# Performance work log

Hardware: AMD Instinct MI355X
Metric: run time of the kernel (lower is better)

## Reference

```python
import jax, jax.numpy as jnp
import numpy as np

VOCAB = 50257
DIM = 1024
B, S = 4, 4096


def setup_inputs() -> dict:
    key = jax.random.key(0)
    k1, k2, k3 = jax.random.split(key, 3)
    input_ids = jax.random.randint(k1, (B, S), 0, VOCAB)
    weight = jax.random.normal(k2, (VOCAB, DIM), dtype=jnp.float32)
    # R initialized as a random matrix stand-in for the learned Stiefel rotation
    R = jax.random.normal(k3, (DIM, DIM), dtype=jnp.float32) / np.sqrt(DIM)
    return {"input_ids": input_ids, "weight": weight, "R": R}


def reference(input_ids, weight, R):
    # Faithful to the module: rotate the FULL embedding table, then gather.
    w_eff = weight @ R              # [V, D] @ [D, D] -> [V, D]
    return jnp.take(w_eff, input_ids, axis=0)  # [B, S, D]
```

## Files before the change

kernel.cpp:

```cpp
#include <hip/hip_runtime.h>
#include <hip/hip_bf16.h>


typedef __attribute__((ext_vector_type(4))) float f32x4;
typedef __attribute__((ext_vector_type(8))) short s16x8;
typedef __attribute__((ext_vector_type(2))) int i32x2;

#define DIM 1024
#define NT 16

__device__ __forceinline__ short f2bf(float f) {
  unsigned u = __float_as_uint(f);
  unsigned r = (u + 0x7FFFu + ((u >> 16) & 1u)) >> 16;
  return (short)r;
}

__device__ __forceinline__ void gload_lds16(const void* g, void* l) {
  __builtin_amdgcn_global_load_lds((const __attribute__((address_space(1))) void*)g,
                                   (__attribute__((address_space(3))) void*)l, 16, 0, 0);
}

__global__ __launch_bounds__(256) void prep_kernel(const float* __restrict__ R,
                                                   short* __restrict__ RT,
                                                   const float* __restrict__ W,
                                                   const int* __restrict__ ids,
                                                   short* __restrict__ G) {
  const int b = blockIdx.x;
  const int t = threadIdx.x;
  if (b < 1024) {
    __shared__ float tile[32][33];
    const int bx = b & 31, by = b >> 5;
    const int tx = t & 31, ty = t >> 5;
#pragma unroll
    for (int i = 0; i < 4; ++i)
      tile[ty + i * 8][tx] = R[(size_t)(by * 32 + ty + i * 8) * DIM + bx * 32 + tx];
    __syncthreads();
#pragma unroll
    for (int i = 0; i < 4; ++i)
      RT[(size_t)(bx * 32 + ty + i * 8) * DIM + by * 32 + tx] = f2bf(tile[tx][ty + i * 8]);
  } else {
    const int tid = (b - 1024) * 256 + t;
#pragma unroll
    for (int i = 0; i < 8; ++i) {
      const int g = tid + i * (2048 * 256);
      const int row = g >> 8;
      const int c4 = (g & 255) << 2;
      const f32x4 v = *(const f32x4*)(W + (size_t)ids[row] * DIM + c4);
      i32x2 p;
      p[0] = (int)(unsigned short)f2bf(v[0]) | ((int)f2bf(v[1]) << 16);
      p[1] = (int)(unsigned short)f2bf(v[2]) | ((int)f2bf(v[3]) << 16);
      *(i32x2*)(G + (size_t)g * 4) = p;
    }
  }
}

__global__ __launch_bounds__(512, 2) void rot_embed_gemm(const short* __restrict__ G,
                                                         const short* __restrict__ RT,
                                                         float* __restrict__ out) {
  extern __shared__ char smem[];

  const int t = threadIdx.x;
  const int b = blockIdx.x;
  const int swz = (b & 7) * 32 + (b >> 3);
  const int m0 = (swz >> 2) * 256;
  const int n0 = (swz & 3) * 256;

  const int lane = t & 63;
  const int w = t >> 6;
  const int wm = w >> 2, wn = w & 3;
  const int fr = lane & 15, fq = lane >> 4;

  char* const ldsA = smem;
  char* const ldsB = smem + 98304;

  const int srow = w * 8 + (lane >> 3);
  const int sch = ((lane & 7) ^ (lane >> 3)) * 8;
  const short* gA = G + (size_t)(m0 + srow) * DIM + sch;
  const short* gB = RT + (size_t)(n0 + srow) * DIM + sch;
  const int ldsOff = w * 1024;

#define STA(buf, kt)                                                        \
  {                                                                         \
    _Pragma("unroll") for (int j = 0; j < 4; ++j)                           \
        gload_lds16(gA + (size_t)j * 64 * DIM + (kt) * 64,                  \
                    ldsA + (buf) * 32768 + j * 8192 + ldsOff);              \
  }
#define STB(buf, kt)                                                        \
  {                                                                         \
    _Pragma("unroll") for (int j = 0; j < 4; ++j)                           \
        gload_lds16(gB + (size_t)j * 64 * DIM + (kt) * 64,                  \
                    ldsB + (buf) * 32768 + j * 8192 + ldsOff);              \
  }

  f32x4 acc[8][4];
#pragma unroll
  for (int i = 0; i < 8; ++i)
#pragma unroll
    for (int j = 0; j < 4; ++j) acc[i][j] = (f32x4)0.0f;

  STA(0, 0);
  STB(0, 0);
  STA(1, 1);

  int bA = 0, bB = 0;
  for (int kt = 0; kt < NT; ++kt) {
    if (kt == NT - 1)
      asm volatile("s_waitcnt vmcnt(0)" ::: "memory");
    else
      asm volatile("s_waitcnt vmcnt(4)" ::: "memory");
    asm volatile("s_waitcnt lgkmcnt(0)" ::: "memory");
    __builtin_amdgcn_s_barrier();

    if (kt + 1 < NT) STB(bB ^ 1, kt + 1);
    if (kt + 2 < NT) { const int nb = (bA + 2 >= 3) ? bA - 1 : bA + 2; STA(nb, kt + 2); }

    const char* A = ldsA + bA * 32768;
    const char* B = ldsB + bB * 32768;
#pragma unroll
    for (int kk = 0; kk < 2; ++kk) {
      const int sl = ((fq + 4 * kk) ^ (fr & 7)) << 4;
      s16x8 af[8], bfv[4];
#pragma unroll
      for (int mi = 0; mi < 8; ++mi)
        af[mi] = *(const s16x8*)(A + (wm * 128 + mi * 16 + fr) * 128 + sl);
#pragma unroll
      for (int nj = 0; nj < 4; ++nj)
        bfv[nj] = *(const s16x8*)(B + (wn * 64 + nj * 16 + fr) * 128 + sl);
      __builtin_amdgcn_s_setprio(1);
#pragma unroll
      for (int mi = 0; mi < 8; ++mi)
#pragma unroll
        for (int nj = 0; nj < 4; ++nj)
          acc[mi][nj] = __builtin_amdgcn_mfma_f32_16x16x32_bf16(af[mi], bfv[nj], acc[mi][nj], 0, 0, 0);
      __builtin_amdgcn_s_setprio(0);
    }

    bA = (bA + 1 == 3) ? 0 : bA + 1;
    bB ^= 1;
  }

#pragma unroll
  for (int mi = 0; mi < 8; ++mi)
#pragma unroll
    for (int nj = 0; nj < 4; ++nj) {
      float* op = out + (size_t)(m0 + wm * 128 + mi * 16 + fq * 4) * DIM +
                  (n0 + wn * 64 + nj * 16 + fr);
#pragma unroll
      for (int r = 0; r < 4; ++r) op[(size_t)r * DIM] = acc[mi][nj][r];
    }
#undef STA
#undef STB
}

extern "C" void kernel_launch(void* const* d_in, const int* in_sizes, int n_in,
                              void* d_out, int out_size, void* d_ws, size_t ws_size,
                              hipStream_t stream) {
  const int* ids = (const int*)d_in[0];
  const float* W = (const float*)d_in[1];
  const float* R = (const float*)d_in[2];
  float* out = (float*)d_out;
  short* RT = (short*)d_ws;
  short* G = (short*)d_ws + (size_t)DIM * DIM;

  prep_kernel<<<dim3(3072), dim3(256), 0, stream>>>(R, RT, W, ids, G);
  rot_embed_gemm<<<dim3(256), dim3(512), 163840, stream>>>(G, RT, out);
}
```

Baseline: 57.42 us.

## Fuse embedding gather and bf16 conversion into GEMM A-tile loading

Removes the separate gather pass that wrote a bf16 copy of the gathered embedding rows. The GEMM now loads fp32 rows of W straight into LDS via global_load_lds, using token ids cached in shared memory, and converts them to bf16 in registers before the MFMAs. The K tile shrinks to 32 with a uniform 3-stage buffer ring and a separate R transpose kernel. This drops the intermediate write and read of G, but doubles A-tile LDS traffic per element, adds convert instructions to the inner loop, and doubles the K-loop iteration count and barriers.

```diff
diff --git a/kernel.cpp b/kernel.cpp
--- a/kernel.cpp
+++ b/kernel.cpp
@@ -3,11 +3,11 @@
 
 
 typedef __attribute__((ext_vector_type(4))) float f32x4;
+typedef __attribute__((ext_vector_type(4))) int i32x4;
 typedef __attribute__((ext_vector_type(8))) short s16x8;
-typedef __attribute__((ext_vector_type(2))) int i32x2;
 
 #define DIM 1024
-#define NT 16
+#define NT 32
 
 __device__ __forceinline__ short f2bf(float f) {
   unsigned u = __float_as_uint(f);
@@ -15,48 +15,34 @@
   return (short)r;
 }
 
+__device__ __forceinline__ int cvt2(float a, float b) {
+  __hip_bfloat162 h = __float22bfloat162_rn(float2{a, b});
+  return *reinterpret_cast<int*>(&h);
+}
+
 __device__ __forceinline__ void gload_lds16(const void* g, void* l) {
   __builtin_amdgcn_global_load_lds((const __attribute__((address_space(1))) void*)g,
                                    (__attribute__((address_space(3))) void*)l, 16, 0, 0);
 }
 
-__global__ __launch_bounds__(256) void prep_kernel(const float* __restrict__ R,
-                                                   short* __restrict__ RT,
-                                                   const float* __restrict__ W,
-                                                   const int* __restrict__ ids,
-                                                   short* __restrict__ G) {
-  const int b = blockIdx.x;
-  const int t = threadIdx.x;
-  if (b < 1024) {
-    __shared__ float tile[32][33];
-    const int bx = b & 31, by = b >> 5;
-    const int tx = t & 31, ty = t >> 5;
+__global__ __launch_bounds__(256) void convert_R_kernel(const float* __restrict__ R,
+                                                        short* __restrict__ RT) {
+  __shared__ float tile[32][33];
+  const int bx = blockIdx.x, by = blockIdx.y;
+  const int tx = threadIdx.x, ty = threadIdx.y;
 #pragma unroll
-    for (int i = 0; i < 4; ++i)
-      tile[ty + i * 8][tx] = R[(size_t)(by * 32 + ty + i * 8) * DIM + bx * 32 + tx];
-    __syncthreads();
+  for (int i = 0; i < 4; ++i)
+    tile[ty + i * 8][tx] = R[(size_t)(by * 32 + ty + i * 8) * DIM + bx * 32 + tx];
+  __syncthreads();
 #pragma unroll
-    for (int i = 0; i < 4; ++i)
-      RT[(size_t)(bx * 32 + ty + i * 8) * DIM + by * 32 + tx] = f2bf(tile[tx][ty + i * 8]);
-  } else {
-    const int tid = (b - 1024) * 256 + t;
-#pragma unroll
-    for (int i = 0; i < 8; ++i) {
-      const int g = tid + i * (2048 * 256);
-      const int row = g >> 8;
-      const int c4 = (g & 255) << 2;
-      const f32x4 v = *(const f32x4*)(W + (size_t)ids[row] * DIM + c4);
-      i32x2 p;
-      p[0] = (int)(unsigned short)f2bf(v[0]) | ((int)f2bf(v[1]) << 16);
-      p[1] = (int)(unsigned short)f2bf(v[2]) | ((int)f2bf(v[3]) << 16);
-      *(i32x2*)(G + (size_t)g * 4) = p;
-    }
-  }
+  for (int i = 0; i < 4; ++i)
+    RT[(size_t)(bx * 32 + ty + i * 8) * DIM + by * 32 + tx] = f2bf(tile[tx][ty + i * 8]);
 }
 
-__global__ __launch_bounds__(512, 2) void rot_embed_gemm(const short* __restrict__ G,
-                                                         const short* __restrict__ RT,
-                                                         float* __restrict__ out) {
+__global__ __launch_bounds__(512, 2) void rot_embed_fused(const float* __restrict__ W,
+                                                          const short* __restrict__ RT,
+                                                          const int* __restrict__ ids,
+                                                          float* __restrict__ out) {
   extern __shared__ char smem[];
 
   const int t = threadIdx.x;
@@ -65,6 +51,10 @@
   const int m0 = (swz >> 2) * 256;
   const int n0 = (swz & 3) * 256;
 
+  int* sIds = (int*)(smem + 147456);
+  if (t < 256) sIds[t] = ids[m0 + t];
+  __syncthreads();
+
   const int lane = t & 63;
   const int w = t >> 6;
   const int wm = w >> 2, wn = w & 3;
@@ -72,24 +62,27 @@
 
   char* const ldsA = smem;
   char* const ldsB = smem + 98304;
-
-  const int srow = w * 8 + (lane >> 3);
-  const int sch = ((lane & 7) ^ (lane >> 3)) * 8;
-  const short* gA = G + (size_t)(m0 + srow) * DIM + sch;
-  const short* gB = RT + (size_t)(n0 + srow) * DIM + sch;
   const int ldsOff = w * 1024;
 
-#define STA(buf, kt)                                                        \
-  {                                                                         \
-    _Pragma("unroll") for (int j = 0; j < 4; ++j)                           \
-        gload_lds16(gA + (size_t)j * 64 * DIM + (kt) * 64,                  \
-                    ldsA + (buf) * 32768 + j * 8192 + ldsOff);              \
-  }
-#define STB(buf, kt)                                                        \
-  {                                                                         \
-    _Pragma("unroll") for (int j = 0; j < 4; ++j)                           \
-        gload_lds16(gB + (size_t)j * 64 * DIM + (kt) * 64,                  \
-                    ldsB + (buf) * 32768 + j * 8192 + ldsOff);              \
+  const int cA = ((lane & 7) ^ (lane >> 3)) * 4;
+  const float* gA0 = W + (size_t)sIds[0 * 64 + w * 8 + (lane >> 3)] * DIM + cA;
+  const float* gA1 = W + (size_t)sIds[1 * 64 + w * 8 + (lane >> 3)] * DIM + cA;
+  const float* gA2 = W + (size_t)sIds[2 * 64 + w * 8 + (lane >> 3)] * DIM + cA;
+  const float* gA3 = W + (size_t)sIds[3 * 64 + w * 8 + (lane >> 3)] * DIM + cA;
+
+  const int cB = ((lane & 3) ^ ((lane >> 2) & 3)) * 8;
+  const short* gB0 = RT + (size_t)(n0 + 0 * 128 + w * 16 + (lane >> 2)) * DIM + cB;
+  const short* gB1 = RT + (size_t)(n0 + 1 * 128 + w * 16 + (lane >> 2)) * DIM + cB;
+
+#define STAGE(buf, kt)                                                   \
+  {                                                                      \
+    const int ko = (kt) * 32;                                            \
+    gload_lds16(gA0 + ko, ldsA + (buf) * 32768 + 0 * 8192 + ldsOff);     \
+    gload_lds16(gA1 + ko, ldsA + (buf) * 32768 + 1 * 8192 + ldsOff);     \
+    gload_lds16(gA2 + ko, ldsA + (buf) * 32768 + 2 * 8192 + ldsOff);     \
+    gload_lds16(gA3 + ko, ldsA + (buf) * 32768 + 3 * 8192 + ldsOff);     \
+    gload_lds16(gB0 + ko, ldsB + (buf) * 16384 + 0 * 8192 + ldsOff);     \
+    gload_lds16(gB1 + ko, ldsB + (buf) * 16384 + 1 * 8192 + ldsOff);     \
   }
 
   f32x4 acc[8][4];
@@ -98,34 +91,46 @@
 #pragma unroll
     for (int j = 0; j < 4; ++j) acc[i][j] = (f32x4)0.0f;
 
-  STA(0, 0);
-  STB(0, 0);
-  STA(1, 1);
+  const int xA = fr & 7;
+  const int s0 = ((2 * fq) ^ xA) << 4;
+  const int s1 = ((2 * fq + 1) ^ xA) << 4;
+  const int sB = (fq ^ (fr & 3)) << 4;
 
-  int bA = 0, bB = 0;
+  STAGE(0, 0);
+  STAGE(1, 1);
+
+  int b0 = 0, b1 = 1, b2 = 2;
   for (int kt = 0; kt < NT; ++kt) {
-    if (kt == NT - 1)
+    if (kt < NT - 1)
+      asm volatile("s_waitcnt vmcnt(6)" ::: "memory");
+    else
       asm volatile("s_waitcnt vmcnt(0)" ::: "memory");
-    else
-      asm volatile("s_waitcnt vmcnt(4)" ::: "memory");
     asm volatile("s_waitcnt lgkmcnt(0)" ::: "memory");
     __builtin_amdgcn_s_barrier();
 
-    if (kt + 1 < NT) STB(bB ^ 1, kt + 1);
-    if (kt + 2 < NT) { const int nb = (bA + 2 >= 3) ? bA - 1 : bA + 2; STA(nb, kt + 2); }
+    if (kt + 2 < NT) STAGE(b2, kt + 2);
 
-    const char* A = ldsA + bA * 32768;
-    const char* B = ldsB + bB * 32768;
-#pragma unroll
-    for (int kk = 0; kk < 2; ++kk) {
-      const int sl = ((fq + 4 * kk) ^ (fr & 7)) << 4;
+    {
+      const char* A = ldsA + b0 * 32768;
+      const char* B = ldsB + b0 * 16384;
       s16x8 af[8], bfv[4];
 #pragma unroll
-      for (int mi = 0; mi < 8; ++mi)
-        af[mi] = *(const s16x8*)(A + (wm * 128 + mi * 16 + fr) * 128 + sl);
+      for (int mi = 0; mi < 8; ++mi) {
+        const int rbase = (wm * 128 + mi * 16 + fr) * 128;
+        const f32x4 lo = *(const f32x4*)(A + rbase + s0);
+        const f32x4 hi = *(const f32x4*)(A + rbase + s1);
+        i32x4 v;
+        v[0] = cvt2(lo[0], lo[1]);
+        v[1] = cvt2(lo[2], lo[3]);
+        v[2] = cvt2(hi[0], hi[1]);
+        v[3] = cvt2(hi[2], hi[3]);
+        af[mi] = *(s16x8*)&v;
+      }
 #pragma unroll
-      for (int nj = 0; nj < 4; ++nj)
-        bfv[nj] = *(const s16x8*)(B + (wn * 64 + nj * 16 + fr) * 128 + sl);
+      for (int nj = 0; nj < 4; ++nj) {
+        const int rb = wn * 64 + nj * 16 + fr;
+        bfv[nj] = *(const s16x8*)(B + rb * 64 + sB);
+      }
       __builtin_amdgcn_s_setprio(1);
 #pragma unroll
       for (int mi = 0; mi < 8; ++mi)
@@ -135,8 +140,7 @@
       __builtin_amdgcn_s_setprio(0);
     }
 
-    bA = (bA + 1 == 3) ? 0 : bA + 1;
-    bB ^= 1;
+    const int tmp = b0; b0 = b1; b1 = b2; b2 = tmp;
   }
 
 #pragma unroll
@@ -148,8 +152,7 @@
 #pragma unroll
       for (int r = 0; r < 4; ++r) op[(size_t)r * DIM] = acc[mi][nj][r];
     }
-#undef STA
-#undef STB
+#undef STAGE
 }
 
 extern "C" void kernel_launch(void* const* d_in, const int* in_sizes, int n_in,
@@ -160,8 +163,7 @@
   const float* R = (const float*)d_in[2];
   float* out = (float*)d_out;
   short* RT = (short*)d_ws;
-  short* G = (short*)d_ws + (size_t)DIM * DIM;
 
-  prep_kernel<<<dim3(3072), dim3(256), 0, stream>>>(R, RT, W, ids, G);
-  rot_embed_gemm<<<dim3(256), dim3(512), 163840, stream>>>(G, RT, out);
+  convert_R_kernel<<<dim3(32, 32), dim3(32, 8), 0, stream>>>(R, RT);
+  rot_embed_fused<<<dim3(256), dim3(512), 148480, stream>>>(W, RT, ids, out);
 }
```

Result: slower. 62.67 us (+9.1%).

## Shrink GEMM tile to 128x256 with BK=32 for more blocks and occupancy

Applied to the files above, without the earlier changes.

The rotation GEMM moves from 256x256 tiles with a K-step of 64 to 128x256 tiles with a K-step of 32. This doubles the grid to 512 blocks, cuts LDS use so more blocks can fit per CU, and raises the launch bounds to allow that. It also drops the s_setprio hints and writes the output with nontemporal stores. The trade-off is less data reuse per tile, twice as many barrier-synchronised K iterations, and fewer MFMAs between each barrier.

```diff
diff --git a/kernel.cpp b/kernel.cpp
--- a/kernel.cpp
+++ b/kernel.cpp
@@ -7,7 +7,7 @@
 typedef __attribute__((ext_vector_type(2))) int i32x2;
 
 #define DIM 1024
-#define NT 16
+#define NTK 32
 
 __device__ __forceinline__ short f2bf(float f) {
   unsigned u = __float_as_uint(f);
@@ -54,15 +54,15 @@
   }
 }
 
-__global__ __launch_bounds__(512, 2) void rot_embed_gemm(const short* __restrict__ G,
+__global__ __launch_bounds__(512, 4) void rot_embed_gemm(const short* __restrict__ G,
                                                          const short* __restrict__ RT,
                                                          float* __restrict__ out) {
   extern __shared__ char smem[];
 
   const int t = threadIdx.x;
   const int b = blockIdx.x;
-  const int swz = (b & 7) * 32 + (b >> 3);
-  const int m0 = (swz >> 2) * 256;
+  const int swz = (b & 7) * 64 + (b >> 3);
+  const int m0 = (swz >> 2) * 128;
   const int n0 = (swz & 3) * 256;
 
   const int lane = t & 63;
@@ -71,82 +71,73 @@
   const int fr = lane & 15, fq = lane >> 4;
 
   char* const ldsA = smem;
-  char* const ldsB = smem + 98304;
+  char* const ldsB = smem + 24576;
 
-  const int srow = w * 8 + (lane >> 3);
-  const int sch = ((lane & 7) ^ (lane >> 3)) * 8;
-  const short* gA = G + (size_t)(m0 + srow) * DIM + sch;
-  const short* gB = RT + (size_t)(n0 + srow) * DIM + sch;
-  const int ldsOff = w * 1024;
+  const int arow = t >> 2;
+  const int achk = ((t & 3) ^ (arow & 3)) * 8;
+  const short* gA = G + (size_t)(m0 + arow) * DIM + achk;
+  const short* gB0 = RT + (size_t)(n0 + arow) * DIM + achk;
+  const short* gB1 = RT + (size_t)(n0 + 128 + arow) * DIM + achk;
+  const int dOff = w * 1024;
 
-#define STA(buf, kt)                                                        \
-  {                                                                         \
-    _Pragma("unroll") for (int j = 0; j < 4; ++j)                           \
-        gload_lds16(gA + (size_t)j * 64 * DIM + (kt) * 64,                  \
-                    ldsA + (buf) * 32768 + j * 8192 + ldsOff);              \
-  }
-#define STB(buf, kt)                                                        \
-  {                                                                         \
-    _Pragma("unroll") for (int j = 0; j < 4; ++j)                           \
-        gload_lds16(gB + (size_t)j * 64 * DIM + (kt) * 64,                  \
-                    ldsB + (buf) * 32768 + j * 8192 + ldsOff);              \
+#define STA(buf, kt) gload_lds16(gA + (kt) * 32, ldsA + (buf) * 8192 + dOff)
+#define STB(buf, kt)                                                   \
+  {                                                                    \
+    gload_lds16(gB0 + (kt) * 32, ldsB + (buf) * 16384 + dOff);         \
+    gload_lds16(gB1 + (kt) * 32, ldsB + (buf) * 16384 + 8192 + dOff);  \
   }
 
-  f32x4 acc[8][4];
+  f32x4 acc[4][4];
 #pragma unroll
-  for (int i = 0; i < 8; ++i)
+  for (int i = 0; i < 4; ++i)
 #pragma unroll
     for (int j = 0; j < 4; ++j) acc[i][j] = (f32x4)0.0f;
+
+  const int sl = (fq ^ (fr & 3)) << 4;
 
   STA(0, 0);
   STB(0, 0);
   STA(1, 1);
 
   int bA = 0, bB = 0;
-  for (int kt = 0; kt < NT; ++kt) {
-    if (kt == NT - 1)
+  for (int kt = 0; kt < NTK; ++kt) {
+    if (kt == NTK - 1)
       asm volatile("s_waitcnt vmcnt(0)" ::: "memory");
     else
-      asm volatile("s_waitcnt vmcnt(4)" ::: "memory");
+      asm volatile("s_waitcnt vmcnt(1)" ::: "memory");
     asm volatile("s_waitcnt lgkmcnt(0)" ::: "memory");
     __builtin_amdgcn_s_barrier();
 
-    if (kt + 1 < NT) STB(bB ^ 1, kt + 1);
-    if (kt + 2 < NT) { const int nb = (bA + 2 >= 3) ? bA - 1 : bA + 2; STA(nb, kt + 2); }
+    if (kt + 1 < NTK) STB(bB ^ 1, kt + 1);
+    if (kt + 2 < NTK) { const int nb = (bA + 2 >= 3) ? bA - 1 : bA + 2; STA(nb, kt + 2); }
 
-    const char* A = ldsA + bA * 32768;
-    const char* B = ldsB + bB * 32768;
+    const char* A = ldsA + bA * 8192;
+    const char* B = ldsB + bB * 16384;
+    s16x8 af[4], bfv[4];
 #pragma unroll
-    for (int kk = 0; kk < 2; ++kk) {
-      const int sl = ((fq + 4 * kk) ^ (fr & 7)) << 4;
-      s16x8 af[8], bfv[4];
+    for (int i = 0; i < 4; ++i) {
+      af[i] = *(const s16x8*)(A + (wm * 64 + i * 16 + fr) * 64 + sl);
+      bfv[i] = *(const s16x8*)(B + (wn * 64 + i * 16 + fr) * 64 + sl);
+    }
 #pragma unroll
-      for (int mi = 0; mi < 8; ++mi)
-        af[mi] = *(const s16x8*)(A + (wm * 128 + mi * 16 + fr) * 128 + sl);
+    for (int mi = 0; mi < 4; ++mi)
 #pragma unroll
       for (int nj = 0; nj < 4; ++nj)
-        bfv[nj] = *(const s16x8*)(B + (wn * 64 + nj * 16 + fr) * 128 + sl);
-      __builtin_amdgcn_s_setprio(1);
-#pragma unroll
-      for (int mi = 0; mi < 8; ++mi)
-#pragma unroll
-        for (int nj = 0; nj < 4; ++nj)
-          acc[mi][nj] = __builtin_amdgcn_mfma_f32_16x16x32_bf16(af[mi], bfv[nj], acc[mi][nj], 0, 0, 0);
-      __builtin_amdgcn_s_setprio(0);
-    }
+        acc[mi][nj] = __builtin_amdgcn_mfma_f32_16x16x32_bf16(af[mi], bfv[nj], acc[mi][nj], 0, 0, 0);
 
     bA = (bA + 1 == 3) ? 0 : bA + 1;
     bB ^= 1;
   }
 
 #pragma unroll
-  for (int mi = 0; mi < 8; ++mi)
+  for (int mi = 0; mi < 4; ++mi)
 #pragma unroll
     for (int nj = 0; nj < 4; ++nj) {
-      float* op = out + (size_t)(m0 + wm * 128 + mi * 16 + fq * 4) * DIM +
+      float* op = out + (size_t)(m0 + wm * 64 + mi * 16 + fq * 4) * DIM +
                   (n0 + wn * 64 + nj * 16 + fr);
 #pragma unroll
-      for (int r = 0; r < 4; ++r) op[(size_t)r * DIM] = acc[mi][nj][r];
+      for (int r = 0; r < 4; ++r)
+        __builtin_nontemporal_store(acc[mi][nj][r], op + (size_t)r * DIM);
     }
 #undef STA
 #undef STB
@@ -163,5 +154,5 @@
   short* G = (short*)d_ws + (size_t)DIM * DIM;
 
   prep_kernel<<<dim3(3072), dim3(256), 0, stream>>>(R, RT, W, ids, G);
-  rot_embed_gemm<<<dim3(256), dim3(512), 163840, stream>>>(G, RT, out);
+  rot_embed_gemm<<<dim3(512), dim3(512), 57344, stream>>>(G, RT, out);
 }
```

Result: slower. 67.54 us (+17.6%).

## Interleave LDS fragment loads, async global loads and MFMA in four phased sub-steps

Applied to the files above, without the earlier changes.

Restructures the GEMM main loop into four phases per K tile. Each phase loads half the A fragments, issues a slice of the next tiles' global-to-LDS copies, then runs a 16-MFMA cluster between barriers. This spreads memory issue across the compute, lowers fragment register pressure (4 A fragments instead of 8), and coordinates the two waves per SIMD so one computes while the other loads. It adds many more barriers per tile, which may cost synchronisation overhead. Output stores are also switched to nontemporal stores.

```diff
diff --git a/kernel.cpp b/kernel.cpp
--- a/kernel.cpp
+++ b/kernel.cpp
@@ -79,18 +79,41 @@
   const short* gB = RT + (size_t)(n0 + srow) * DIM + sch;
   const int ldsOff = w * 1024;
 
-#define STA(buf, kt)                                                        \
+#define STA2(buf, kt, j0)                                                   \
   {                                                                         \
-    _Pragma("unroll") for (int j = 0; j < 4; ++j)                           \
-        gload_lds16(gA + (size_t)j * 64 * DIM + (kt) * 64,                  \
-                    ldsA + (buf) * 32768 + j * 8192 + ldsOff);              \
+    gload_lds16(gA + (size_t)(j0) * 64 * DIM + (kt) * 64,                   \
+                ldsA + (buf) * 32768 + (j0) * 8192 + ldsOff);               \
+    gload_lds16(gA + (size_t)((j0) + 1) * 64 * DIM + (kt) * 64,             \
+                ldsA + (buf) * 32768 + ((j0) + 1) * 8192 + ldsOff);         \
   }
-#define STB(buf, kt)                                                        \
+#define STB2(buf, kt, j0)                                                   \
   {                                                                         \
-    _Pragma("unroll") for (int j = 0; j < 4; ++j)                           \
-        gload_lds16(gB + (size_t)j * 64 * DIM + (kt) * 64,                  \
-                    ldsB + (buf) * 32768 + j * 8192 + ldsOff);              \
+    gload_lds16(gB + (size_t)(j0) * 64 * DIM + (kt) * 64,                   \
+                ldsB + (buf) * 32768 + (j0) * 8192 + ldsOff);               \
+    gload_lds16(gB + (size_t)((j0) + 1) * 64 * DIM + (kt) * 64,             \
+                ldsB + (buf) * 32768 + ((j0) + 1) * 8192 + ldsOff);         \
   }
+#define LDA4(A, rowbase, sl)                                                \
+  {                                                                         \
+    _Pragma("unroll") for (int i = 0; i < 4; ++i)                           \
+        af[i] = *(const s16x8*)((A) + ((rowbase) + i * 16 + fr) * 128 + (sl)); \
+  }
+#define LDB4(B, sl)                                                         \
+  {                                                                         \
+    _Pragma("unroll") for (int i = 0; i < 4; ++i)                           \
+        bfv[i] = *(const s16x8*)((B) + (wn * 64 + i * 16 + fr) * 128 + (sl)); \
+  }
+#define MFMA16(h)                                                           \
+  {                                                                         \
+    __builtin_amdgcn_s_setprio(1);                                          \
+    _Pragma("unroll") for (int mi = 0; mi < 4; ++mi)                        \
+        _Pragma("unroll") for (int nj = 0; nj < 4; ++nj)                    \
+            acc[(h) * 4 + mi][nj] = __builtin_amdgcn_mfma_f32_16x16x32_bf16( \
+                af[mi], bfv[nj], acc[(h) * 4 + mi][nj], 0, 0, 0);           \
+    __builtin_amdgcn_s_setprio(0);                                          \
+  }
+#define BAR __builtin_amdgcn_s_barrier()
+#define LGKM0 asm volatile("s_waitcnt lgkmcnt(0)" ::: "memory")
 
   f32x4 acc[8][4];
 #pragma unroll
@@ -98,45 +121,48 @@
 #pragma unroll
     for (int j = 0; j < 4; ++j) acc[i][j] = (f32x4)0.0f;
 
-  STA(0, 0);
-  STB(0, 0);
-  STA(1, 1);
+  STA2(0, 0, 0); STA2(0, 0, 2);
+  STB2(0, 0, 0); STB2(0, 0, 2);
+  STA2(1, 1, 0); STA2(1, 1, 2);
+  asm volatile("s_waitcnt vmcnt(4)" ::: "memory");
+  BAR;
 
-  int bA = 0, bB = 0;
   for (int kt = 0; kt < NT; ++kt) {
-    if (kt == NT - 1)
+    const char* A = ldsA + (kt % 3) * 32768;
+    const char* B = ldsB + (kt & 1) * 32768;
+    const int sl0 = (fq ^ (fr & 7)) << 4;
+    const int sl1 = ((fq + 4) ^ (fr & 7)) << 4;
+    s16x8 af[4], bfv[4];
+
+    LDA4(A, wm * 128, sl0);
+    LDB4(B, sl0);
+    if (kt + 1 < NT) STB2((kt + 1) & 1, kt + 1, 0);
+    BAR; LGKM0;
+    MFMA16(0);
+    BAR;
+
+    LDA4(A, wm * 128 + 64, sl0);
+    if (kt + 1 < NT) STB2((kt + 1) & 1, kt + 1, 2);
+    BAR; LGKM0;
+    MFMA16(1);
+    BAR;
+
+    LDA4(A, wm * 128, sl1);
+    LDB4(B, sl1);
+    if (kt + 2 < NT) STA2((kt + 2) % 3, kt + 2, 0);
+    BAR; LGKM0;
+    MFMA16(0);
+    BAR;
+
+    LDA4(A, wm * 128 + 64, sl1);
+    if (kt + 2 < NT) STA2((kt + 2) % 3, kt + 2, 2);
+    if (kt + 2 < NT)
+      asm volatile("s_waitcnt vmcnt(4)" ::: "memory");
+    else if (kt + 1 < NT)
       asm volatile("s_waitcnt vmcnt(0)" ::: "memory");
-    else
-      asm volatile("s_waitcnt vmcnt(4)" ::: "memory");
-    asm volatile("s_waitcnt lgkmcnt(0)" ::: "memory");
-    __builtin_amdgcn_s_barrier();
-
-    if (kt + 1 < NT) STB(bB ^ 1, kt + 1);
-    if (kt + 2 < NT) { const int nb = (bA + 2 >= 3) ? bA - 1 : bA + 2; STA(nb, kt + 2); }
-
-    const char* A = ldsA + bA * 32768;
-    const char* B = ldsB + bB * 32768;
-#pragma unroll
-    for (int kk = 0; kk < 2; ++kk) {
-      const int sl = ((fq + 4 * kk) ^ (fr & 7)) << 4;
-      s16x8 af[8], bfv[4];
-#pragma unroll
-      for (int mi = 0; mi < 8; ++mi)
-        af[mi] = *(const s16x8*)(A + (wm * 128 + mi * 16 + fr) * 128 + sl);
-#pragma unroll
-      for (int nj = 0; nj < 4; ++nj)
-        bfv[nj] = *(const s16x8*)(B + (wn * 64 + nj * 16 + fr) * 128 + sl);
-      __builtin_amdgcn_s_setprio(1);
-#pragma unroll
-      for (int mi = 0; mi < 8; ++mi)
-#pragma unroll
-        for (int nj = 0; nj < 4; ++nj)
-          acc[mi][nj] = __builtin_amdgcn_mfma_f32_16x16x32_bf16(af[mi], bfv[nj], acc[mi][nj], 0, 0, 0);
-      __builtin_amdgcn_s_setprio(0);
-    }
-
-    bA = (bA + 1 == 3) ? 0 : bA + 1;
-    bB ^= 1;
+    BAR; LGKM0;
+    MFMA16(1);
+    BAR;
   }
 
 #pragma unroll
@@ -146,10 +172,16 @@
       float* op = out + (size_t)(m0 + wm * 128 + mi * 16 + fq * 4) * DIM +
                   (n0 + wn * 64 + nj * 16 + fr);
 #pragma unroll
-      for (int r = 0; r < 4; ++r) op[(size_t)r * DIM] = acc[mi][nj][r];
+      for (int r = 0; r < 4; ++r)
+        __builtin_nontemporal_store(acc[mi][nj][r], op + (size_t)r * DIM);
     }
-#undef STA
-#undef STB
+#undef STA2
+#undef STB2
+#undef LDA4
+#undef LDB4
+#undef MFMA16
+#undef BAR
+#undef LGKM0
 }
 
 extern "C" void kernel_launch(void* const* d_in, const int* in_sizes, int n_in,
```

New measurement: 64.26 us. 11.9% more time.
